# Kernel optimization log

Measured on AMD Instinct MI355X. Metric: run time of the kernel, lower is better.

The kernel has to match this reference:

```python
import jax, jax.numpy as jnp
import numpy as np

N, B, NPG, E = 16384, 64, 256, 524288
F_IN, POS_DIM, L_PE = 32, 3, 8
W, HEADS, LAYERS, DFF = 256, 8, 2, 1024
HID, OUT = 512, 64
S = NPG + 1
DH = W // HEADS


def _ln(x, s, b, eps=1e-5):
    m = jnp.mean(x, -1, keepdims=True)
    v = jnp.var(x, -1, keepdims=True)
    return (x - m) * jax.lax.rsqrt(v + eps) * s + b


def _gelu(x):
    # custom tanh-approx GELU from the source module
    c = float(np.sqrt(2.0 / np.pi))
    return 0.5 * x * (1.0 + jnp.tanh(c * (x + 0.044715 * x ** 3)))


def setup_inputs() -> dict:
    key = jax.random.key(0)
    ks = jax.random.split(key, 24)
    nrm = lambda k, shape, s=0.05: jax.random.normal(k, shape, jnp.float32) * s
    D_IN = F_IN + POS_DIM * L_PE  # 56
    inp = {}
    inp['x'] = jax.random.normal(ks[0], (N, F_IN), jnp.float32)
    inp['p'] = jax.random.uniform(ks[1], (N, POS_DIM), jnp.float32, -1.0, 1.0)
    inp['edge_index'] = jax.random.randint(ks[2], (2, E), 0, N, jnp.int32)
    inp['batch'] = (jnp.arange(N) // NPG).astype(jnp.int32)  # sorted, 64 equal graphs
    inp['gcn_w'] = nrm(ks[3], (D_IN, W), 0.1)
    inp['gcn_b'] = jnp.zeros((W,), jnp.float32)
    inp['cls_token'] = nrm(ks[4], (1, 1, W), 0.02)
    inp['ln_pre_s'] = jnp.ones((W,), jnp.float32)
    inp['ln_pre_b'] = jnp.zeros((W,), jnp.float32)
    inp['norm1_s'] = jnp.ones((LAYERS, W), jnp.float32)
    inp['norm1_b'] = jnp.zeros((LAYERS, W), jnp.float32)
    inp['in_proj_w'] = nrm(ks[5], (LAYERS, W, 3 * W))
    inp['in_proj_b'] = jnp.zeros((LAYERS, 3 * W), jnp.float32)
    inp['out_proj_w'] = nrm(ks[6], (LAYERS, W, W))
    inp['out_proj_b'] = jnp.zeros((LAYERS, W), jnp.float32)
    inp['norm2_s'] = jnp.ones((LAYERS, W), jnp.float32)
    inp['norm2_b'] = jnp.zeros((LAYERS, W), jnp.float32)
    inp['ff_w1'] = nrm(ks[7], (LAYERS, W, DFF))
    inp['ff_b1'] = jnp.zeros((LAYERS, DFF), jnp.float32)
    inp['ff_w2'] = nrm(ks[8], (LAYERS, DFF, W))
    inp['ff_b2'] = jnp.zeros((LAYERS, W), jnp.float32)
    inp['ln_post_s'] = jnp.ones((W,), jnp.float32)
    inp['ln_post_b'] = jnp.zeros((W,), jnp.float32)
    inp['dec_w1'] = nrm(ks[9], (W, HID))
    inp['dec_b1'] = jnp.zeros((HID,), jnp.float32)
    inp['dec_w2'] = nrm(ks[10], (HID, HID))
    inp['dec_b2'] = jnp.zeros((HID,), jnp.float32)
    inp['dec_w3'] = nrm(ks[11], (HID, OUT))
    inp['dec_b3'] = jnp.zeros((OUT,), jnp.float32)
    return inp


def _forward(x, p, gcn_w, gcn_b, cls_token, ln_pre_s, ln_pre_b, norm1_s, norm1_b,
             in_proj_w, in_proj_b, out_proj_w, out_proj_b, norm2_s, norm2_b,
             ff_w1, ff_b1, ff_w2, ff_b2, ln_post_s, ln_post_b,
             dec_w1, dec_b1, dec_w2, dec_b2, dec_w3, dec_b3, edge_index, batch):
    # positional encoding: sin(p * 2^i * pi), i = 0..L-1
    freqs = (2.0 ** jnp.arange(L_PE, dtype=jnp.float32)) * jnp.pi
    pe = jnp.sin(p[:, :, None] * freqs).reshape(N, POS_DIM * L_PE)
    xc = jnp.concatenate([x, pe], axis=-1)  # [N, 56]
    # GCNConv: x W, then sym-normalized aggregation with self loops, + bias
    xw = xc @ gcn_w  # [N, W]
    loop = jnp.arange(N, dtype=edge_index.dtype)
    row = jnp.concatenate([edge_index[0], loop])
    col = jnp.concatenate([edge_index[1], loop])
    deg = jax.ops.segment_sum(jnp.ones_like(row, dtype=xw.dtype), col, num_segments=N)
    dinv = jax.lax.rsqrt(jnp.maximum(deg, 1e-12))
    coef = dinv[row] * dinv[col]
    h = jax.ops.segment_sum(coef[:, None] * xw[row], col, num_segments=N) + gcn_b
    # to_dense_batch (batch is sorted graph ids)
    counts = jax.ops.segment_sum(jnp.ones((N,), jnp.int32), batch, num_segments=B)
    ptr = jnp.concatenate([jnp.zeros((1,), jnp.int32), jnp.cumsum(counts)[:-1]])
    pos = jnp.arange(N, dtype=jnp.int32) - ptr[batch]
    dense = jnp.zeros((B, NPG, W), h.dtype).at[batch, pos].set(h)
    mask = jnp.zeros((B, NPG), bool).at[batch, pos].set(True)
    # prepend cls token
    xd = jnp.concatenate([jnp.broadcast_to(cls_token, (B, 1, W)), dense], axis=1)  # [B,S,W]
    valid = jnp.concatenate([jnp.ones((B, 1), bool), mask], axis=1)  # [B,S]
    xd = _ln(xd, ln_pre_s, ln_pre_b)
    # causal mask with row 0 (cls) unmasked
    am = jnp.triu(jnp.ones((S, S), bool), k=1)
    am = am.at[0, :].set(False)
    allowed = (~am)[None, :, :] & valid[:, None, :]  # [B,S,S]
    scale = 1.0 / float(np.sqrt(DH))
    for l in range(LAYERS):
        h1 = _ln(xd, norm1_s[l], norm1_b[l])
        qkv = h1 @ in_proj_w[l] + in_proj_b[l]  # [B,S,3W]
        q, k, v = jnp.split(qkv, 3, axis=-1)
        q = q.reshape(B, S, HEADS, DH)
        k = k.reshape(B, S, HEADS, DH)
        v = v.reshape(B, S, HEADS, DH)
        sc = jnp.einsum('bqhd,bkhd->bhqk', q, k) * scale
        sc = jnp.where(allowed[:, None, :, :], sc, -1e9)
        a = jax.nn.softmax(sc, axis=-1)
        o = jnp.einsum('bhqk,bkhd->bqhd', a, v).reshape(B, S, W)
        xd = xd + (o @ out_proj_w[l] + out_proj_b[l])
        h2 = _ln(xd, norm2_s[l], norm2_b[l])
        # MLP(num_layers=2) applies activation after BOTH layers (incl. last)
        ff = _gelu(_gelu(h2 @ ff_w1[l] + ff_b1[l]) @ ff_w2[l] + ff_b2[l])
        xd = xd + ff
    cls = _ln(xd[:, 0, :], ln_post_s, ln_post_b)
    # decoder MLP(num_layers=3) with relu after every layer (incl. last)
    h3 = jax.nn.relu(cls @ dec_w1 + dec_b1)
    h3 = jax.nn.relu(h3 @ dec_w2 + dec_b2)
    return jax.nn.relu(h3 @ dec_w3 + dec_b3)


def reference(x, p, gcn_w, gcn_b, cls_token, ln_pre_s, ln_pre_b, norm1_s, norm1_b,
              in_proj_w, in_proj_b, out_proj_w, out_proj_b, norm2_s, norm2_b,
              ff_w1, ff_b1, ff_w2, ff_b2, ln_post_s, ln_post_b,
              dec_w1, dec_b1, dec_w2, dec_b2, dec_w3, dec_b3, edge_index, batch):
    return _forward(x, p, gcn_w, gcn_b, cls_token, ln_pre_s, ln_pre_b, norm1_s, norm1_b,
                    in_proj_w, in_proj_b, out_proj_w, out_proj_b, norm2_s, norm2_b,
                    ff_w1, ff_b1, ff_w2, ff_b2, ln_post_s, ln_post_b,
                    dec_w1, dec_b1, dec_w2, dec_b2, dec_w3, dec_b3, edge_index, batch)
```

## Files before the change

### kernel.cpp

```cpp
#include <hip/hip_runtime.h>
#include <math.h>

constexpr int N_NODES = 16384;
constexpr int BGRAPH  = 64;
constexpr int NEDGE   = 524288;
constexpr int SEQ     = 257;
constexpr int WDIM    = 256;
constexpr int DFF     = 1024;
constexpr int HID     = 512;
constexpr int MROWS   = BGRAPH * SEQ;

constexpr size_t F_Y    = 0;
constexpr size_t F_AGG  = F_Y    + (size_t)N_NODES * 64;
constexpr size_t F_XD   = F_AGG  + (size_t)N_NODES * 64;
constexpr size_t F_CLS  = F_XD   + (size_t)MROWS * WDIM;
constexpr size_t F_D1   = F_CLS  + (size_t)BGRAPH * WDIM;
constexpr size_t F_D2   = F_D1   + (size_t)BGRAPH * HID;
constexpr size_t F_WPAD = F_D2   + (size_t)BGRAPH * HID;
constexpr size_t F_DINV = F_WPAD + (size_t)64 * WDIM;
constexpr size_t F_IEND = F_DINV + (size_t)N_NODES;

typedef __attribute__((ext_vector_type(8))) __bf16 bf16x8;
typedef __attribute__((ext_vector_type(4))) __bf16 bf16x4;
typedef __attribute__((ext_vector_type(4))) float f32x4;

__device__ __forceinline__ float gelu_f(float x) {
    float u = 0.7978845608028654f * (x + 0.044715f * x * x * x);
    return 0.5f * x * (1.0f + tanhf(u));
}

__global__ __launch_bounds__(256) void hist_kernel(const int* __restrict__ col, int* __restrict__ indeg) {
    int e = blockIdx.x * 256 + threadIdx.x;
    atomicAdd(&indeg[col[e]], 1);
}

__global__ __launch_bounds__(1024) void scan_kernel(const int* __restrict__ indeg, int* __restrict__ offs,
                                                    int* __restrict__ cursor, float* __restrict__ dinv) {
    __shared__ int parts[1024];
    int t = threadIdx.x;
    int base = t * 16;
    int loc[16];
    int s = 0;
#pragma unroll
    for (int i = 0; i < 16; ++i) { loc[i] = indeg[base + i]; s += loc[i]; }
    parts[t] = s;
    __syncthreads();
    for (int off = 1; off < 1024; off <<= 1) {
        int v = (t >= off) ? parts[t - off] : 0;
        __syncthreads();
        parts[t] += v;
        __syncthreads();
    }
    int run = (t == 0) ? 0 : parts[t - 1];
#pragma unroll
    for (int i = 0; i < 16; ++i) {
        offs[base + i] = run;
        cursor[base + i] = run;
        dinv[base + i] = rsqrtf((float)loc[i] + 1.0f);
        run += loc[i];
    }
    if (t == 1023) offs[N_NODES] = run;
}

__global__ __launch_bounds__(256) void fill_kernel(const int* __restrict__ ei, int* __restrict__ cursor,
                                                   int* __restrict__ csr) {
    int e = blockIdx.x * 256 + threadIdx.x;
    int r = ei[e];
    int c = ei[NEDGE + e];
    int pos = atomicAdd(&cursor[c], 1);
    csr[pos] = r;
}

__global__ __launch_bounds__(256) void y_kernel(const float* __restrict__ x, const float* __restrict__ p,
                                                const float* __restrict__ dinv, float* __restrict__ y) {
    int idx = blockIdx.x * 256 + threadIdx.x;
    int i = idx >> 6, d = idx & 63;
    float v = 0.f;
    if (d < 32) {
        v = x[i * 32 + d];
    } else if (d < 56) {
        int dd = d - 32;
        int dim = dd >> 3, j = dd & 7;
        v = sinf(p[i * 3 + dim] * (3.14159265358979323846f * (float)(1 << j)));
    }
    y[idx] = dinv[i] * v;
}

__global__ __launch_bounds__(256) void agg_kernel(const float* __restrict__ y, const float* __restrict__ dinv,
                                                  const int* __restrict__ offs, const int* __restrict__ csr,
                                                  float* __restrict__ agg) {
    int c = (blockIdx.x * 256 + threadIdx.x) >> 6;
    int lane = threadIdx.x & 63;
    float acc = y[(size_t)c * 64 + lane];
    int s = offs[c], e = offs[c + 1];
    for (int j = s; j < e; ++j) {
        int r = csr[j];
        acc += y[(size_t)r * 64 + lane];
    }
    agg[(size_t)c * 64 + lane] = dinv[c] * acc;
}

__global__ __launch_bounds__(256) void wpad_kernel(const float* __restrict__ w, float* __restrict__ wp) {
    int idx = blockIdx.x * 256 + threadIdx.x;
    wp[idx] = (idx < 56 * 256) ? w[idx] : 0.f;
}

__global__ __launch_bounds__(256) void cls_write(const float* __restrict__ tok, float* __restrict__ xd) {
    xd[(size_t)blockIdx.x * SEQ * WDIM + threadIdx.x] = tok[threadIdx.x];
}

template <int OUTBF>
__global__ __launch_bounds__(256) void ln4_kernel(const float* __restrict__ in, int rin_stride,
                                                  void* __restrict__ out,
                                                  const float* __restrict__ g, const float* __restrict__ be) {
    int w = threadIdx.x >> 6, lane = threadIdx.x & 63;
    int row = blockIdx.x * 4 + w;
    const float* ip = in + (size_t)row * rin_stride + lane * 4;
    f32x4 v = *(const f32x4*)ip;
    float s = v[0] + v[1] + v[2] + v[3];
    float ss = v[0] * v[0] + v[1] * v[1] + v[2] * v[2] + v[3] * v[3];
#pragma unroll
    for (int off = 1; off < 64; off <<= 1) { s += __shfl_xor(s, off); ss += __shfl_xor(ss, off); }
    float mean = s * 0.00390625f;
    float var = ss * 0.00390625f - mean * mean;
    float rs = rsqrtf(var + 1e-5f);
    f32x4 gv = *(const f32x4*)(g + lane * 4);
    f32x4 bv = *(const f32x4*)(be + lane * 4);
    if (OUTBF) {
        bf16x4 o;
#pragma unroll
        for (int i = 0; i < 4; ++i) o[i] = (__bf16)((v[i] - mean) * rs * gv[i] + bv[i]);
        *(bf16x4*)((__bf16*)out + (size_t)row * 256 + lane * 4) = o;
    } else {
        f32x4 o;
#pragma unroll
        for (int i = 0; i < 4; ++i) o[i] = (v[i] - mean) * rs * gv[i] + bv[i];
        *(f32x4*)((float*)out + (size_t)row * 256 + lane * 4) = o;
    }
}

__global__ __launch_bounds__(256) void tcast_kernel(const float* __restrict__ W, __bf16* __restrict__ Wt,
                                                    int K, int N) {
    __shared__ __bf16 T[64][65];
    int t = threadIdx.x;
    int k0 = blockIdx.x << 6, n0 = blockIdx.y << 6;
#pragma unroll
    for (int i = 0; i < 16; ++i) {
        int idx = t + i * 256;
        int k = idx >> 6, n = idx & 63;
        T[k][n] = (__bf16)W[(size_t)(k0 + k) * N + n0 + n];
    }
    __syncthreads();
#pragma unroll
    for (int i = 0; i < 16; ++i) {
        int idx = t + i * 256;
        int n = idx >> 6, k = idx & 63;
        Wt[(size_t)(n0 + n) * K + k0 + k] = T[k][n];
    }
}

constexpr int LP = 36;
template <int BN, int ACT, int OMODE>
__global__ __launch_bounds__(256) void gemm_bf(const __bf16* __restrict__ A, int lda,
                                               const __bf16* __restrict__ Bt,
                                               const float* __restrict__ bias,
                                               void* __restrict__ Cv, int ldc,
                                               int Ktot, int Mrows, int MBlocks, int NY) {
    constexpr int NTW = BN / 32;
    __shared__ __bf16 As[128 * LP];
    __shared__ __bf16 Bs[BN * LP];
    int f = blockIdx.x;
    int m8 = f & 7;
    int rest = f >> 3;
    int mg = rest / NY;
    int yb = rest - mg * NY;
    int mb = mg * 8 + m8;
    if (mb >= MBlocks) return;
    int m0 = mb << 7, n0 = yb * BN;

    int t = threadIdx.x;
    int w = t >> 6, L = t & 63;
    int wm = w >> 1, wn = w & 1;
    int lc = L & 15, quad = L >> 4;

    int sa_row = t >> 1, sa_off = (t & 1) << 4;
    const __bf16* ap = A + (size_t)(m0 + sa_row) * lda + sa_off;
    __bf16* as_dst = &As[sa_row * LP + sa_off];
    const __bf16* bp;
    __bf16* bs_dst;
    if constexpr (BN == 128) {
        bp = Bt + (size_t)(n0 + sa_row) * Ktot + sa_off;
        bs_dst = &Bs[sa_row * LP + sa_off];
    } else {
        int sb_row = t >> 2, sb_off = (t & 3) << 3;
        bp = Bt + (size_t)(n0 + sb_row) * Ktot + sb_off;
        bs_dst = &Bs[sb_row * LP + sb_off];
    }

    int a_base = (wm * 64 + lc) * LP + quad * 8;
    int b_base = (wn * (BN / 2) + lc) * LP + quad * 8;

    f32x4 acc[4][NTW] = {};

    bf16x8 a0 = *(const bf16x8*)(ap);
    bf16x8 a1 = *(const bf16x8*)(ap + 8);
    bf16x8 b0, b1;
    if constexpr (BN == 128) {
        b0 = *(const bf16x8*)(bp);
        b1 = *(const bf16x8*)(bp + 8);
    } else {
        b0 = *(const bf16x8*)(bp);
    }

    for (int k0 = 0; k0 < Ktot; k0 += 32) {
        __syncthreads();
        *(bf16x8*)as_dst = a0;
        *(bf16x8*)(as_dst + 8) = a1;
        if constexpr (BN == 128) {
            *(bf16x8*)bs_dst = b0;
            *(bf16x8*)(bs_dst + 8) = b1;
        } else {
            *(bf16x8*)bs_dst = b0;
        }
        __syncthreads();
        if (k0 + 32 < Ktot) {
            a0 = *(const bf16x8*)(ap + k0 + 32);
            a1 = *(const bf16x8*)(ap + k0 + 40);
            if constexpr (BN == 128) {
                b0 = *(const bf16x8*)(bp + k0 + 32);
                b1 = *(const bf16x8*)(bp + k0 + 40);
            } else {
                b0 = *(const bf16x8*)(bp + k0 + 32);
            }
        }
        bf16x8 af[4], bfr[NTW];
#pragma unroll
        for (int i = 0; i < 4; ++i) af[i] = *(const bf16x8*)&As[a_base + i * 16 * LP];
#pragma unroll
        for (int i = 0; i < NTW; ++i) bfr[i] = *(const bf16x8*)&Bs[b_base + i * 16 * LP];
#pragma unroll
        for (int mt = 0; mt < 4; ++mt)
#pragma unroll
            for (int nt = 0; nt < NTW; ++nt)
                acc[mt][nt] = __builtin_amdgcn_mfma_f32_16x16x32_bf16(af[mt], bfr[nt], acc[mt][nt], 0, 0, 0);
    }

#pragma unroll
    for (int mt = 0; mt < 4; ++mt) {
        int gmb = m0 + wm * 64 + mt * 16 + quad * 4;
#pragma unroll
        for (int nt = 0; nt < NTW; ++nt) {
            int gn = n0 + wn * (BN / 2) + nt * 16 + lc;
            float bv = bias[gn];
#pragma unroll
            for (int r = 0; r < 4; ++r) {
                int gm = gmb + r;
                if (gm >= Mrows) continue;
                float v = acc[mt][nt][r] + bv;
                if (ACT == 1) v = gelu_f(v);
                if (OMODE == 0) {
                    ((__bf16*)Cv)[(size_t)gm * ldc + gn] = (__bf16)v;
                } else {
                    float* cp = (float*)Cv + (size_t)gm * ldc + gn;
                    *cp = v + *cp;
                }
            }
        }
    }
}

constexpr int PPITCH = 280;
__global__ __launch_bounds__(256, 2) void attn_mfma(const __bf16* __restrict__ qkvb,
                                                    __bf16* __restrict__ obuf) {
    __shared__ __bf16 Vt[32][PPITCH];
    __shared__ __bf16 Pb[4][16][PPITCH];
    int bb = blockIdx.x;
    int b = bb >> 3, h = bb & 7;
    int t = threadIdx.x;
    int w = t >> 6, L = t & 63;
    int c = L & 15, quad = L >> 4;
    const float scale = 0.17677669529663687f;
    const __bf16* qb = qkvb + (size_t)(b * SEQ) * 768 + h * 32;
    const __bf16* kb = qb + 256;
    const __bf16* vb = qb + 512;
    __bf16* ob = obuf + (size_t)(b * SEQ) * 256 + h * 32;

    for (int idx = t; idx < 272 * 4; idx += 256) {
        int key = idx >> 2, dc = (idx & 3) * 8;
        bf16x8 vv = {};
        if (key < SEQ) vv = *(const bf16x8*)(vb + (size_t)key * 768 + dc);
#pragma unroll
        for (int j = 0; j < 8; ++j) Vt[dc + j][key] = vv[j];
    }
    __syncthreads();

#pragma unroll 1
    for (int qt = 0; qt < 5; ++qt) {
        int q0 = qt * 64 + w * 16;
        if (q0 > 256) continue;
        int ntiles = (qt == 0 && w == 0) ? 17 : (qt * 4 + w + 1);
        if (ntiles > 17) ntiles = 17;
        int nkc = (ntiles + 1) >> 1;

        bf16x8 qf;
        {
            int qr = q0 + c; if (qr > 256) qr = 256;
            qf = *(const bf16x8*)(qb + (size_t)qr * 768 + quad * 8);
        }

        f32x4 acc[17];
#pragma unroll
        for (int tt = 0; tt < 17; ++tt) {
            if (tt >= ntiles) continue;
            int kr = tt * 16 + c; if (kr > 256) kr = 256;
            bf16x8 kf = *(const bf16x8*)(kb + (size_t)kr * 768 + quad * 8);
            f32x4 z = {0.f, 0.f, 0.f, 0.f};
            acc[tt] = __builtin_amdgcn_mfma_f32_16x16x32_bf16(qf, kf, z, 0, 0, 0);
        }

        float inv[4];
#pragma unroll
        for (int j = 0; j < 4; ++j) {
            int q = q0 + quad * 4 + j;
            float mx = -3.0e38f;
#pragma unroll
            for (int tt = 0; tt < 17; ++tt) {
                if (tt >= ntiles) continue;
                int key = tt * 16 + c;
                bool ok = (key < SEQ) && (q == 0 || key <= q);
                float v = ok ? acc[tt][j] * scale : -3.0e38f;
                mx = fmaxf(mx, v);
            }
            mx = fmaxf(mx, __shfl_xor(mx, 1));
            mx = fmaxf(mx, __shfl_xor(mx, 2));
            mx = fmaxf(mx, __shfl_xor(mx, 4));
            mx = fmaxf(mx, __shfl_xor(mx, 8));
            float s = 0.f;
#pragma unroll
            for (int tt = 0; tt < 17; ++tt) {
                if (tt >= ntiles) continue;
                int key = tt * 16 + c;
                bool ok = (key < SEQ) && (q == 0 || key <= q);
                float pv = ok ? expf(acc[tt][j] * scale - mx) : 0.f;
                s += pv;
                Pb[w][quad * 4 + j][key] = (__bf16)pv;
            }
            if ((ntiles & 1) && ntiles < 17)
                Pb[w][quad * 4 + j][ntiles * 16 + c] = (__bf16)0.f;
            s += __shfl_xor(s, 1);
            s += __shfl_xor(s, 2);
            s += __shfl_xor(s, 4);
            s += __shfl_xor(s, 8);
            inv[j] = 1.0f / s;
        }

        f32x4 oacc0 = {0.f, 0.f, 0.f, 0.f};
        f32x4 oacc1 = {0.f, 0.f, 0.f, 0.f};
#pragma unroll
        for (int kc = 0; kc < 9; ++kc) {
            if (kc >= nkc) continue;
            int off = kc * 32 + quad * 8;
            bf16x8 af = {};
            bf16x8 bf0 = {};
            bf16x8 bf1 = {};
            if (off < 257) {
                af  = *(const bf16x8*)&Pb[w][c][off];
                bf0 = *(const bf16x8*)&Vt[c][off];
                bf1 = *(const bf16x8*)&Vt[16 + c][off];
            }
            oacc0 = __builtin_amdgcn_mfma_f32_16x16x32_bf16(af, bf0, oacc0, 0, 0, 0);
            oacc1 = __builtin_amdgcn_mfma_f32_16x16x32_bf16(af, bf1, oacc1, 0, 0, 0);
        }

#pragma unroll
        for (int j = 0; j < 4; ++j) {
            int q = q0 + quad * 4 + j;
            if (q < SEQ) {
                __bf16* op = ob + (size_t)q * 256;
                op[c]      = (__bf16)(oacc0[j] * inv[j]);
                op[16 + c] = (__bf16)(oacc1[j] * inv[j]);
            }
        }
    }
}

template <int ACT, bool RESID, bool REMAP>
__global__ __launch_bounds__(256) void gemm_std(const float* __restrict__ A, int lda,
                                                const float* __restrict__ Bw, int ldb,
                                                const float* __restrict__ bias,
                                                float* __restrict__ C, int ldc, int Ktot) {
    int t = threadIdx.x;
    int m0 = blockIdx.x << 6, n0 = blockIdx.y << 6;
    __shared__ float As[16][68];
    __shared__ float Bs[16][64];
    int arow = t >> 2, akk = (t & 3) << 2;
    int bk = t >> 4, bn = (t & 15) << 2;
    int tm = (t >> 4) << 2, tn = (t & 15) << 2;
    float acc[4][4] = {};
    const float* ap = A + (size_t)(m0 + arow) * lda + akk;
    const float* bp = Bw + (size_t)bk * ldb + n0 + bn;
    for (int k0 = 0; k0 < Ktot; k0 += 16) {
        float4 av = *(const float4*)(ap + k0);
        float4 bv = *(const float4*)(bp + (size_t)k0 * ldb);
        __syncthreads();
        As[akk + 0][arow] = av.x; As[akk + 1][arow] = av.y;
        As[akk + 2][arow] = av.z; As[akk + 3][arow] = av.w;
        *(float4*)&Bs[bk][bn] = bv;
        __syncthreads();
#pragma unroll
        for (int k = 0; k < 16; ++k) {
            float4 a = *(const float4*)&As[k][tm];
            float4 b = *(const float4*)&Bs[k][tn];
            acc[0][0] += a.x * b.x; acc[0][1] += a.x * b.y; acc[0][2] += a.x * b.z; acc[0][3] += a.x * b.w;
            acc[1][0] += a.y * b.x; acc[1][1] += a.y * b.y; acc[1][2] += a.y * b.z; acc[1][3] += a.y * b.w;
            acc[2][0] += a.z * b.x; acc[2][1] += a.z * b.y; acc[2][2] += a.z * b.z; acc[2][3] += a.z * b.w;
            acc[3][0] += a.w * b.x; acc[3][1] += a.w * b.y; acc[3][2] += a.w * b.z; acc[3][3] += a.w * b.w;
        }
    }
#pragma unroll
    for (int i = 0; i < 4; ++i) {
        int gm = m0 + tm + i;
        int orow = REMAP ? (gm + (gm >> 8) + 1) : gm;
        float* cp = C + (size_t)orow * ldc + n0 + tn;
        float4 r;
        r.x = acc[i][0] + bias[n0 + tn + 0];
        r.y = acc[i][1] + bias[n0 + tn + 1];
        r.z = acc[i][2] + bias[n0 + tn + 2];
        r.w = acc[i][3] + bias[n0 + tn + 3];
        if (ACT == 1) { r.x = gelu_f(r.x); r.y = gelu_f(r.y); r.z = gelu_f(r.z); r.w = gelu_f(r.w); }
        if (ACT == 2) { r.x = fmaxf(r.x, 0.f); r.y = fmaxf(r.y, 0.f); r.z = fmaxf(r.z, 0.f); r.w = fmaxf(r.w, 0.f); }
        if (RESID) {
            float4 o = *(const float4*)cp;
            r.x += o.x; r.y += o.y; r.z += o.z; r.w += o.w;
        }
        *(float4*)cp = r;
    }
}

template <int K, int NOUT>
__global__ __launch_bounds__(256) void dec_fc2(const float* __restrict__ in, const float* __restrict__ w,
                                               const float* __restrict__ bia, float* __restrict__ out) {
    __shared__ float rowbuf[K];
    __shared__ float part[4][64];
    int b = blockIdx.x, c = blockIdx.y, t = threadIdx.x;
    for (int i = t; i < K; i += 256) rowbuf[i] = in[(size_t)b * K + i];
    __syncthreads();
    int lane = t & 63, wv = t >> 6;
    int n = c * 64 + lane;
    const int KQ = K / 4;
    const float* wp = w + (size_t)(wv * KQ) * NOUT + n;
    float s = 0.f;
#pragma unroll 8
    for (int k = 0; k < KQ; ++k) s += rowbuf[wv * KQ + k] * wp[(size_t)k * NOUT];
    part[wv][lane] = s;
    __syncthreads();
    if (wv == 0) {
        float r = part[0][lane] + part[1][lane] + part[2][lane] + part[3][lane] + bia[n];
        out[(size_t)b * NOUT + n] = fmaxf(r, 0.f);
    }
}

extern "C" void kernel_launch(void* const* d_in, const int* in_sizes, int n_in,
                              void* d_out, int out_size, void* d_ws, size_t ws_size,
                              hipStream_t stream) {
    const float* x         = (const float*)d_in[0];
    const float* p         = (const float*)d_in[1];
    const int*   ei        = (const int*)d_in[2];
    const float* gcn_w     = (const float*)d_in[4];
    const float* gcn_b     = (const float*)d_in[5];
    const float* cls_tok   = (const float*)d_in[6];
    const float* ln_pre_s  = (const float*)d_in[7];
    const float* ln_pre_b  = (const float*)d_in[8];
    const float* norm1_s   = (const float*)d_in[9];
    const float* norm1_b   = (const float*)d_in[10];
    const float* in_proj_w = (const float*)d_in[11];
    const float* in_proj_b = (const float*)d_in[12];
    const float* out_proj_w= (const float*)d_in[13];
    const float* out_proj_b= (const float*)d_in[14];
    const float* norm2_s   = (const float*)d_in[15];
    const float* norm2_b   = (const float*)d_in[16];
    const float* ff_w1     = (const float*)d_in[17];
    const float* ff_b1     = (const float*)d_in[18];
    const float* ff_w2     = (const float*)d_in[19];
    const float* ff_b2     = (const float*)d_in[20];
    const float* ln_post_s = (const float*)d_in[21];
    const float* ln_post_b = (const float*)d_in[22];
    const float* dec_w1    = (const float*)d_in[23];
    const float* dec_b1    = (const float*)d_in[24];
    const float* dec_w2    = (const float*)d_in[25];
    const float* dec_b2    = (const float*)d_in[26];
    const float* dec_w3    = (const float*)d_in[27];
    const float* dec_b3    = (const float*)d_in[28];

    float* ws   = (float*)d_ws;
    float* y    = ws + F_Y;
    float* agg  = ws + F_AGG;
    float* xd   = ws + F_XD;
    float* cls  = ws + F_CLS;
    float* dd1  = ws + F_D1;
    float* dd2  = ws + F_D2;
    float* wpad = ws + F_WPAD;
    float* dinv = ws + F_DINV;
    int* ibase  = (int*)(ws + F_IEND);
    int* indeg  = ibase;
    int* offs   = ibase + N_NODES;
    int* cursor = offs + N_NODES + 1;
    int* csr    = cursor + N_NODES;
    uintptr_t ub = ((uintptr_t)(csr + NEDGE) + 15) & ~(uintptr_t)15;
    __bf16* h1b  = (__bf16*)ub;
    __bf16* qkvb = h1b  + (size_t)MROWS * 256;
    __bf16* ffbb = qkvb + (size_t)MROWS * 768;
    __bf16* wt_in  = ffbb  + (size_t)MROWS * 1024;
    __bf16* wt_out = wt_in  + 2 * 768 * 256;
    __bf16* wt_f1  = wt_out + 2 * 256 * 256;
    __bf16* wt_f2  = wt_f1  + 2 * 1024 * 256;

    hipMemsetAsync(indeg, 0, N_NODES * sizeof(int), stream);
    hist_kernel<<<NEDGE / 256, 256, 0, stream>>>(ei + NEDGE, indeg);
    scan_kernel<<<1, 1024, 0, stream>>>(indeg, offs, cursor, dinv);
    fill_kernel<<<NEDGE / 256, 256, 0, stream>>>(ei, cursor, csr);
    y_kernel<<<N_NODES * 64 / 256, 256, 0, stream>>>(x, p, dinv, y);
    agg_kernel<<<N_NODES / 4, 256, 0, stream>>>(y, dinv, offs, csr, agg);
    wpad_kernel<<<64, 256, 0, stream>>>(gcn_w, wpad);

    for (int l = 0; l < 2; ++l) {
        tcast_kernel<<<dim3(4, 12), 256, 0, stream>>>(in_proj_w + (size_t)l * 256 * 768,
                                                      wt_in + (size_t)l * 768 * 256, 256, 768);
        tcast_kernel<<<dim3(4, 4), 256, 0, stream>>>(out_proj_w + (size_t)l * 256 * 256,
                                                     wt_out + (size_t)l * 256 * 256, 256, 256);
        tcast_kernel<<<dim3(4, 16), 256, 0, stream>>>(ff_w1 + (size_t)l * 256 * 1024,
                                                      wt_f1 + (size_t)l * 1024 * 256, 256, 1024);
        tcast_kernel<<<dim3(16, 4), 256, 0, stream>>>(ff_w2 + (size_t)l * 1024 * 256,
                                                      wt_f2 + (size_t)l * 256 * 1024, 1024, 256);
    }

    gemm_std<0, false, true><<<dim3(256, 4), 256, 0, stream>>>(agg, 64, wpad, 256, gcn_b, xd, 256, 64);
    cls_write<<<64, 256, 0, stream>>>(cls_tok, xd);
    ln4_kernel<0><<<MROWS / 4, 256, 0, stream>>>(xd, 256, xd, ln_pre_s, ln_pre_b);

    const int MB = (MROWS + 127) / 128;
    const int MG8 = (MB + 7) / 8;
    for (int l = 0; l < 2; ++l) {
        ln4_kernel<1><<<MROWS / 4, 256, 0, stream>>>(xd, 256, h1b, norm1_s + l * WDIM, norm1_b + l * WDIM);
        gemm_bf<128, 0, 0><<<8 * 6 * MG8, 256, 0, stream>>>(
            h1b, 256, wt_in + (size_t)l * 768 * 256, in_proj_b + l * 768, qkvb, 768, 256, MROWS, MB, 6);
        attn_mfma<<<512, 256, 0, stream>>>(qkvb, h1b);
        gemm_bf<64, 0, 1><<<8 * 4 * MG8, 256, 0, stream>>>(
            h1b, 256, wt_out + (size_t)l * 256 * 256, out_proj_b + l * WDIM, xd, 256, 256, MROWS, MB, 4);
        ln4_kernel<1><<<MROWS / 4, 256, 0, stream>>>(xd, 256, h1b, norm2_s + l * WDIM, norm2_b + l * WDIM);
        gemm_bf<128, 1, 0><<<8 * 8 * MG8, 256, 0, stream>>>(
            h1b, 256, wt_f1 + (size_t)l * 1024 * 256, ff_b1 + l * DFF, ffbb, 1024, 256, MROWS, MB, 8);
        gemm_bf<64, 1, 1><<<8 * 4 * MG8, 256, 0, stream>>>(
            ffbb, 1024, wt_f2 + (size_t)l * 256 * 1024, ff_b2 + l * WDIM, xd, 256, 1024, MROWS, MB, 4);
    }

    ln4_kernel<0><<<BGRAPH / 4, 256, 0, stream>>>(xd, SEQ * WDIM, cls, ln_post_s, ln_post_b);
    dec_fc2<256, 512><<<dim3(BGRAPH, 8), 256, 0, stream>>>(cls, dec_w1, dec_b1, dd1);
    dec_fc2<512, 512><<<dim3(BGRAPH, 8), 256, 0, stream>>>(dd1, dec_w2, dec_b2, dd2);
    dec_fc2<512, 64><<<dim3(BGRAPH, 1), 256, 0, stream>>>(dd2, dec_w3, dec_b3, (float*)d_out);
}
```

Measured before the change: 741.5 us.

## Replace LDS-staged bf16 GEMM with direct-to-register MFMA fragment loads

The transformer GEMM no longer stages A and B tiles through shared memory with two barriers per k-step. Each wave now loads its MFMA fragments straight from global memory into registers, double-buffered, and the out_proj and ff2 GEMMs move to 128-wide N tiles. Separately, attention preloads all 17 K fragments into registers once per block instead of reloading them for every query tile. This removes LDS traffic and synchronisation, but tiles shared across waves are now fetched redundantly from global or L2 memory, and register pressure rises.

Result: slower. 957.9 us (+29.2%).

```diff
diff --git a/kernel.cpp b/kernel.cpp
--- a/kernel.cpp
+++ b/kernel.cpp
@@ -159,16 +159,12 @@
     }
 }
 
-constexpr int LP = 36;
-template <int BN, int ACT, int OMODE>
-__global__ __launch_bounds__(256) void gemm_bf(const __bf16* __restrict__ A, int lda,
+template <int ACT, int OMODE>
+__global__ __launch_bounds__(256) void gemm_dx(const __bf16* __restrict__ A, int lda,
                                                const __bf16* __restrict__ Bt,
                                                const float* __restrict__ bias,
                                                void* __restrict__ Cv, int ldc,
                                                int Ktot, int Mrows, int MBlocks, int NY) {
-    constexpr int NTW = BN / 32;
-    __shared__ __bf16 As[128 * LP];
-    __shared__ __bf16 Bs[BN * LP];
     int f = blockIdx.x;
     int m8 = f & 7;
     int rest = f >> 3;
@@ -176,81 +172,48 @@
     int yb = rest - mg * NY;
     int mb = mg * 8 + m8;
     if (mb >= MBlocks) return;
-    int m0 = mb << 7, n0 = yb * BN;
+    int m0 = mb << 7, n0 = yb << 7;
 
     int t = threadIdx.x;
     int w = t >> 6, L = t & 63;
     int wm = w >> 1, wn = w & 1;
     int lc = L & 15, quad = L >> 4;
 
-    int sa_row = t >> 1, sa_off = (t & 1) << 4;
-    const __bf16* ap = A + (size_t)(m0 + sa_row) * lda + sa_off;
-    __bf16* as_dst = &As[sa_row * LP + sa_off];
-    const __bf16* bp;
-    __bf16* bs_dst;
-    if constexpr (BN == 128) {
-        bp = Bt + (size_t)(n0 + sa_row) * Ktot + sa_off;
-        bs_dst = &Bs[sa_row * LP + sa_off];
-    } else {
-        int sb_row = t >> 2, sb_off = (t & 3) << 3;
-        bp = Bt + (size_t)(n0 + sb_row) * Ktot + sb_off;
-        bs_dst = &Bs[sb_row * LP + sb_off];
-    }
-
-    int a_base = (wm * 64 + lc) * LP + quad * 8;
-    int b_base = (wn * (BN / 2) + lc) * LP + quad * 8;
-
-    f32x4 acc[4][NTW] = {};
-
-    bf16x8 a0 = *(const bf16x8*)(ap);
-    bf16x8 a1 = *(const bf16x8*)(ap + 8);
-    bf16x8 b0, b1;
-    if constexpr (BN == 128) {
-        b0 = *(const bf16x8*)(bp);
-        b1 = *(const bf16x8*)(bp + 8);
-    } else {
-        b0 = *(const bf16x8*)(bp);
-    }
-
+    const __bf16* ap = A + (size_t)(m0 + wm * 64 + lc) * lda + quad * 8;
+    const __bf16* bp = Bt + (size_t)(n0 + wn * 64 + lc) * Ktot + quad * 8;
+    const size_t astep = (size_t)16 * lda;
+    const size_t bstep = (size_t)16 * Ktot;
+
+    f32x4 acc[4][4] = {};
+    bf16x8 a_cur[4], b_cur[4], a_nxt[4], b_nxt[4];
+#pragma unroll
+    for (int i = 0; i < 4; ++i) {
+        a_cur[i] = *(const bf16x8*)(ap + i * astep);
+        b_cur[i] = *(const bf16x8*)(bp + i * bstep);
+    }
     for (int k0 = 0; k0 < Ktot; k0 += 32) {
-        __syncthreads();
-        *(bf16x8*)as_dst = a0;
-        *(bf16x8*)(as_dst + 8) = a1;
-        if constexpr (BN == 128) {
-            *(bf16x8*)bs_dst = b0;
-            *(bf16x8*)(bs_dst + 8) = b1;
-        } else {
-            *(bf16x8*)bs_dst = b0;
-        }
-        __syncthreads();
         if (k0 + 32 < Ktot) {
-            a0 = *(const bf16x8*)(ap + k0 + 32);
-            a1 = *(const bf16x8*)(ap + k0 + 40);
-            if constexpr (BN == 128) {
-                b0 = *(const bf16x8*)(bp + k0 + 32);
-                b1 = *(const bf16x8*)(bp + k0 + 40);
-            } else {
-                b0 = *(const bf16x8*)(bp + k0 + 32);
+#pragma unroll
+            for (int i = 0; i < 4; ++i) {
+                a_nxt[i] = *(const bf16x8*)(ap + i * astep + k0 + 32);
+                b_nxt[i] = *(const bf16x8*)(bp + i * bstep + k0 + 32);
             }
         }
-        bf16x8 af[4], bfr[NTW];
-#pragma unroll
-        for (int i = 0; i < 4; ++i) af[i] = *(const bf16x8*)&As[a_base + i * 16 * LP];
-#pragma unroll
-        for (int i = 0; i < NTW; ++i) bfr[i] = *(const bf16x8*)&Bs[b_base + i * 16 * LP];
 #pragma unroll
         for (int mt = 0; mt < 4; ++mt)
 #pragma unroll
-            for (int nt = 0; nt < NTW; ++nt)
-                acc[mt][nt] = __builtin_amdgcn_mfma_f32_16x16x32_bf16(af[mt], bfr[nt], acc[mt][nt], 0, 0, 0);
+            for (int nt = 0; nt < 4; ++nt)
+                acc[mt][nt] = __builtin_amdgcn_mfma_f32_16x16x32_bf16(a_cur[mt], b_cur[nt], acc[mt][nt], 0, 0, 0);
+#pragma unroll
+        for (int i = 0; i < 4; ++i) { a_cur[i] = a_nxt[i]; b_cur[i] = b_nxt[i]; }
     }
 
 #pragma unroll
     for (int mt = 0; mt < 4; ++mt) {
         int gmb = m0 + wm * 64 + mt * 16 + quad * 4;
 #pragma unroll
-        for (int nt = 0; nt < NTW; ++nt) {
-            int gn = n0 + wn * (BN / 2) + nt * 16 + lc;
+        for (int nt = 0; nt < 4; ++nt) {
+            int gn = n0 + wn * 64 + nt * 16 + lc;
             float bv = bias[gn];
 #pragma unroll
             for (int r = 0; r < 4; ++r) {
@@ -292,6 +255,13 @@
 #pragma unroll
         for (int j = 0; j < 8; ++j) Vt[dc + j][key] = vv[j];
     }
+
+    bf16x8 kfr[17];
+#pragma unroll
+    for (int tt = 0; tt < 17; ++tt) {
+        int kr = tt * 16 + c; if (kr > 256) kr = 256;
+        kfr[tt] = *(const bf16x8*)(kb + (size_t)kr * 768 + quad * 8);
+    }
     __syncthreads();
 
 #pragma unroll 1
@@ -312,10 +282,8 @@
 #pragma unroll
         for (int tt = 0; tt < 17; ++tt) {
             if (tt >= ntiles) continue;
-            int kr = tt * 16 + c; if (kr > 256) kr = 256;
-            bf16x8 kf = *(const bf16x8*)(kb + (size_t)kr * 768 + quad * 8);
             f32x4 z = {0.f, 0.f, 0.f, 0.f};
-            acc[tt] = __builtin_amdgcn_mfma_f32_16x16x32_bf16(qf, kf, z, 0, 0, 0);
+            acc[tt] = __builtin_amdgcn_mfma_f32_16x16x32_bf16(qf, kfr[tt], z, 0, 0, 0);
         }
 
         float inv[4];
@@ -542,16 +510,16 @@
     const int MG8 = (MB + 7) / 8;
     for (int l = 0; l < 2; ++l) {
         ln4_kernel<1><<<MROWS / 4, 256, 0, stream>>>(xd, 256, h1b, norm1_s + l * WDIM, norm1_b + l * WDIM);
-        gemm_bf<128, 0, 0><<<8 * 6 * MG8, 256, 0, stream>>>(
+        gemm_dx<0, 0><<<8 * 6 * MG8, 256, 0, stream>>>(
             h1b, 256, wt_in + (size_t)l * 768 * 256, in_proj_b + l * 768, qkvb, 768, 256, MROWS, MB, 6);
         attn_mfma<<<512, 256, 0, stream>>>(qkvb, h1b);
-        gemm_bf<64, 0, 1><<<8 * 4 * MG8, 256, 0, stream>>>(
-            h1b, 256, wt_out + (size_t)l * 256 * 256, out_proj_b + l * WDIM, xd, 256, 256, MROWS, MB, 4);
+        gemm_dx<0, 1><<<8 * 2 * MG8, 256, 0, stream>>>(
+            h1b, 256, wt_out + (size_t)l * 256 * 256, out_proj_b + l * WDIM, xd, 256, 256, MROWS, MB, 2);
         ln4_kernel<1><<<MROWS / 4, 256, 0, stream>>>(xd, 256, h1b, norm2_s + l * WDIM, norm2_b + l * WDIM);
-        gemm_bf<128, 1, 0><<<8 * 8 * MG8, 256, 0, stream>>>(
+        gemm_dx<1, 0><<<8 * 8 * MG8, 256, 0, stream>>>(
             h1b, 256, wt_f1 + (size_t)l * 1024 * 256, ff_b1 + l * DFF, ffbb, 1024, 256, MROWS, MB, 8);
-        gemm_bf<64, 1, 1><<<8 * 4 * MG8, 256, 0, stream>>>(
-            ffbb, 1024, wt_f2 + (size_t)l * 256 * 1024, ff_b2 + l * WDIM, xd, 256, 1024, MROWS, MB, 4);
+        gemm_dx<1, 1><<<8 * 2 * MG8, 256, 0, stream>>>(
+            ffbb, 1024, wt_f2 + (size_t)l * 256 * 1024, ff_b2 + l * WDIM, xd, 256, 1024, MROWS, MB, 2);
     }
 
     ln4_kernel<0><<<BGRAPH / 4, 256, 0, stream>>>(xd, SEQ * WDIM, cls, ln_post_s, ln_post_b);
```

## Deepen GEMM global prefetch to two stages and hoist K fragments in attention

Applied to the files above, without the earlier changes.

The GEMM main loop now keeps two k-slices of A/B in registers (even and odd) and processes 64 columns per iteration, so each global load is issued roughly two tiles ahead of its use. The attention kernel loads all 17 key fragments into registers once per wave instead of reloading them for every query tile, and the shared-memory pitch is changed from 280 to 284 to shift bank mapping. This raises register pressure (17 extra bf16x8 per thread in attention, doubled staging registers in GEMM), which risks lowering occupancy or causing spills. The unrolled GEMM loop also assumes Ktot is a multiple of 64.

New measurement: 718.5 us. 3.1% less time.

```diff
diff --git a/kernel.cpp b/kernel.cpp
--- a/kernel.cpp
+++ b/kernel.cpp
@@ -202,47 +202,82 @@
 
     f32x4 acc[4][NTW] = {};
 
-    bf16x8 a0 = *(const bf16x8*)(ap);
-    bf16x8 a1 = *(const bf16x8*)(ap + 8);
-    bf16x8 b0, b1;
+    bf16x8 ea0, ea1, eb0, eb1, oa0, oa1, ob0, ob1;
+    ea0 = *(const bf16x8*)(ap);        ea1 = *(const bf16x8*)(ap + 8);
+    oa0 = *(const bf16x8*)(ap + 32);   oa1 = *(const bf16x8*)(ap + 40);
     if constexpr (BN == 128) {
-        b0 = *(const bf16x8*)(bp);
-        b1 = *(const bf16x8*)(bp + 8);
+        eb0 = *(const bf16x8*)(bp);        eb1 = *(const bf16x8*)(bp + 8);
+        ob0 = *(const bf16x8*)(bp + 32);   ob1 = *(const bf16x8*)(bp + 40);
     } else {
-        b0 = *(const bf16x8*)(bp);
-    }
-
-    for (int k0 = 0; k0 < Ktot; k0 += 32) {
-        __syncthreads();
-        *(bf16x8*)as_dst = a0;
-        *(bf16x8*)(as_dst + 8) = a1;
+        eb0 = *(const bf16x8*)(bp);
+        ob0 = *(const bf16x8*)(bp + 32);
+    }
+
+    for (int k0 = 0; k0 < Ktot; k0 += 64) {
+        __syncthreads();
+        *(bf16x8*)as_dst = ea0;
+        *(bf16x8*)(as_dst + 8) = ea1;
         if constexpr (BN == 128) {
-            *(bf16x8*)bs_dst = b0;
-            *(bf16x8*)(bs_dst + 8) = b1;
+            *(bf16x8*)bs_dst = eb0;
+            *(bf16x8*)(bs_dst + 8) = eb1;
         } else {
-            *(bf16x8*)bs_dst = b0;
-        }
-        __syncthreads();
-        if (k0 + 32 < Ktot) {
-            a0 = *(const bf16x8*)(ap + k0 + 32);
-            a1 = *(const bf16x8*)(ap + k0 + 40);
+            *(bf16x8*)bs_dst = eb0;
+        }
+        __syncthreads();
+        if (k0 + 64 < Ktot) {
+            ea0 = *(const bf16x8*)(ap + k0 + 64);
+            ea1 = *(const bf16x8*)(ap + k0 + 72);
             if constexpr (BN == 128) {
-                b0 = *(const bf16x8*)(bp + k0 + 32);
-                b1 = *(const bf16x8*)(bp + k0 + 40);
+                eb0 = *(const bf16x8*)(bp + k0 + 64);
+                eb1 = *(const bf16x8*)(bp + k0 + 72);
             } else {
-                b0 = *(const bf16x8*)(bp + k0 + 32);
+                eb0 = *(const bf16x8*)(bp + k0 + 64);
             }
         }
-        bf16x8 af[4], bfr[NTW];
-#pragma unroll
-        for (int i = 0; i < 4; ++i) af[i] = *(const bf16x8*)&As[a_base + i * 16 * LP];
-#pragma unroll
-        for (int i = 0; i < NTW; ++i) bfr[i] = *(const bf16x8*)&Bs[b_base + i * 16 * LP];
-#pragma unroll
-        for (int mt = 0; mt < 4; ++mt)
-#pragma unroll
-            for (int nt = 0; nt < NTW; ++nt)
-                acc[mt][nt] = __builtin_amdgcn_mfma_f32_16x16x32_bf16(af[mt], bfr[nt], acc[mt][nt], 0, 0, 0);
+        {
+            bf16x8 af[4], bfr[NTW];
+#pragma unroll
+            for (int i = 0; i < 4; ++i) af[i] = *(const bf16x8*)&As[a_base + i * 16 * LP];
+#pragma unroll
+            for (int i = 0; i < NTW; ++i) bfr[i] = *(const bf16x8*)&Bs[b_base + i * 16 * LP];
+#pragma unroll
+            for (int mt = 0; mt < 4; ++mt)
+#pragma unroll
+                for (int nt = 0; nt < NTW; ++nt)
+                    acc[mt][nt] = __builtin_amdgcn_mfma_f32_16x16x32_bf16(af[mt], bfr[nt], acc[mt][nt], 0, 0, 0);
+        }
+        __syncthreads();
+        *(bf16x8*)as_dst = oa0;
+        *(bf16x8*)(as_dst + 8) = oa1;
+        if constexpr (BN == 128) {
+            *(bf16x8*)bs_dst = ob0;
+            *(bf16x8*)(bs_dst + 8) = ob1;
+        } else {
+            *(bf16x8*)bs_dst = ob0;
+        }
+        __syncthreads();
+        if (k0 + 96 < Ktot) {
+            oa0 = *(const bf16x8*)(ap + k0 + 96);
+            oa1 = *(const bf16x8*)(ap + k0 + 104);
+            if constexpr (BN == 128) {
+                ob0 = *(const bf16x8*)(bp + k0 + 96);
+                ob1 = *(const bf16x8*)(bp + k0 + 104);
+            } else {
+                ob0 = *(const bf16x8*)(bp + k0 + 96);
+            }
+        }
+        {
+            bf16x8 af[4], bfr[NTW];
+#pragma unroll
+            for (int i = 0; i < 4; ++i) af[i] = *(const bf16x8*)&As[a_base + i * 16 * LP];
+#pragma unroll
+            for (int i = 0; i < NTW; ++i) bfr[i] = *(const bf16x8*)&Bs[b_base + i * 16 * LP];
+#pragma unroll
+            for (int mt = 0; mt < 4; ++mt)
+#pragma unroll
+                for (int nt = 0; nt < NTW; ++nt)
+                    acc[mt][nt] = __builtin_amdgcn_mfma_f32_16x16x32_bf16(af[mt], bfr[nt], acc[mt][nt], 0, 0, 0);
+        }
     }
 
 #pragma unroll
@@ -269,7 +304,7 @@
     }
 }
 
-constexpr int PPITCH = 280;
+constexpr int PPITCH = 284;
 __global__ __launch_bounds__(256, 2) void attn_mfma(const __bf16* __restrict__ qkvb,
                                                     __bf16* __restrict__ obuf) {
     __shared__ __bf16 Vt[32][PPITCH];
@@ -292,6 +327,13 @@
 #pragma unroll
         for (int j = 0; j < 8; ++j) Vt[dc + j][key] = vv[j];
     }
+
+    bf16x8 kfr[17];
+#pragma unroll
+    for (int tt = 0; tt < 17; ++tt) {
+        int kr = tt * 16 + c; if (kr > 256) kr = 256;
+        kfr[tt] = *(const bf16x8*)(kb + (size_t)kr * 768 + quad * 8);
+    }
     __syncthreads();
 
 #pragma unroll 1
@@ -312,10 +354,8 @@
 #pragma unroll
         for (int tt = 0; tt < 17; ++tt) {
             if (tt >= ntiles) continue;
-            int kr = tt * 16 + c; if (kr > 256) kr = 256;
-            bf16x8 kf = *(const bf16x8*)(kb + (size_t)kr * 768 + quad * 8);
             f32x4 z = {0.f, 0.f, 0.f, 0.f};
-            acc[tt] = __builtin_amdgcn_mfma_f32_16x16x32_bf16(qf, kf, z, 0, 0, 0);
+            acc[tt] = __builtin_amdgcn_mfma_f32_16x16x32_bf16(qf, kfr[tt], z, 0, 0, 0);
         }
 
         float inv[4];
```
